# Performance work log

Hardware: AMD Instinct MI355X
Metric: run time of the kernel (lower is better)

## Reference

```python
import jax, jax.numpy as jnp
import numpy as np

MULTIRES = 6          # positional-encoding frequencies (get_embedder)
SKIP_LAYER = 4        # skip_in=(4,) in ImplicitNetwork
BETA = 100.0          # Softplus(beta=100)
INV_SQRT2 = float(1.0 / np.sqrt(2.0))
NUM_NETS = 64         # multi displacement networks (clusters)


def embed(x):
    """NeRF positional embedding: [x, sin(2^k x), cos(2^k x)] for k=0..MULTIRES-1.
    x: [N,3] -> [N, 3 + 3*2*MULTIRES] = [N,39]."""
    outs = [x]
    for i in range(MULTIRES):
        f = float(2.0 ** i)
        outs.append(jnp.sin(f * x))
        outs.append(jnp.cos(f * x))
    return jnp.concatenate(outs, axis=-1)


def softplus100(x):
    # numerically stable softplus with beta=100
    return jnp.logaddexp(0.0, BETA * x) / BETA


def _forward(points,
             iW0, ib0, iW1, ib1, iW2, ib2, iW3, ib3, iW4, ib4,
             iW5, ib5, iW6, ib6, iW7, ib7, iW8, ib8,
             dW0, db0, dW1, db1, dW2, db2, dW3, db3,
             mW0, mb0, mW1, mb1, mW2, mb2):
    N = points.shape[0]
    inp = embed(points)  # [N,39]

    # ---- ImplicitNetwork: 9 linears, softplus(beta=100), skip concat at l=4 ----
    iWs = [iW0, iW1, iW2, iW3, iW4, iW5, iW6, iW7, iW8]
    ibs = [ib0, ib1, ib2, ib3, ib4, ib5, ib6, ib7, ib8]
    x = inp
    for l in range(9):
        if l == SKIP_LAYER:
            x = jnp.concatenate([x, inp], axis=1) * INV_SQRT2  # [N,473+39=512]
        x = x @ iWs[l].T + ibs[l]
        if l < 8:
            x = softplus100(x)
    sdf_feat = x  # [N,257] = sdf (1) + feature vector (256)

    # ---- DisplacementNetwork: 4 linears, ReLU on hidden, Tanh output ----
    xd = inp
    for W, b, last in ((dW0, db0, False), (dW1, db1, False), (dW2, db2, False), (dW3, db3, True)):
        xd = xd @ W.T + b
        xd = jnp.tanh(xd) if last else jax.nn.relu(xd)
    disp = xd  # [N,3]

    # ---- MultiDisplacementNetwork: batched per-cluster MLPs via bmm ----
    xm = inp.reshape(NUM_NETS, -1, inp.shape[1])  # [n, N/n, 39]
    xm = jax.nn.relu(jnp.einsum('nbi,noi->nbo', xm, mW0) + mb0[:, None, :])
    xm = jax.nn.relu(jnp.einsum('nbi,noi->nbo', xm, mW1) + mb1[:, None, :])
    xm = jnp.tanh(jnp.einsum('nbi,noi->nbo', xm, mW2) + mb2[:, None, :])
    mdisp = xm.reshape(N, 3)

    return jnp.concatenate([sdf_feat, disp, mdisp], axis=1)  # [N, 263]


def setup_inputs() -> dict:
    key = jax.random.key(0)
    ks = iter(jax.random.split(key, 80))
    N = 32768
    d = {}
    d['points'] = jax.random.uniform(next(ks), (N, 3), jnp.float32, -1.0, 1.0)

    def mk(out, inn):
        W = jax.random.normal(next(ks), (out, inn), jnp.float32) * (1.0 / np.sqrt(inn))
        b = jax.random.normal(next(ks), (out,), jnp.float32) * 0.01
        return W, b

    impl_shapes = [(512, 39), (512, 512), (512, 512), (473, 512), (512, 512),
                   (512, 512), (512, 512), (512, 512), (257, 512)]
    for l, (o, i) in enumerate(impl_shapes):
        d[f'iW{l}'], d[f'ib{l}'] = mk(o, i)

    disp_shapes = [(512, 39), (512, 512), (512, 512), (3, 512)]
    for l, (o, i) in enumerate(disp_shapes):
        d[f'dW{l}'], d[f'db{l}'] = mk(o, i)

    multi_shapes = [(128, 39), (128, 128), (3, 128)]
    for l, (o, i) in enumerate(multi_shapes):
        W = jax.random.normal(next(ks), (NUM_NETS, o, i), jnp.float32) * (1.0 / np.sqrt(i))
        b = jax.random.normal(next(ks), (NUM_NETS, o), jnp.float32) * 0.01
        d[f'mW{l}'], d[f'mb{l}'] = W, b
    return d


def reference(points,
              iW0, ib0, iW1, ib1, iW2, ib2, iW3, ib3, iW4, ib4,
              iW5, ib5, iW6, ib6, iW7, ib7, iW8, ib8,
              dW0, db0, dW1, db1, dW2, db2, dW3, db3,
              mW0, mb0, mW1, mb1, mW2, mb2):
    return _forward(points,
                    iW0, ib0, iW1, ib1, iW2, ib2, iW3, ib3, iW4, ib4,
                    iW5, ib5, iW6, ib6, iW7, ib7, iW8, ib8,
                    dW0, db0, dW1, db1, dW2, db2, dW3, db3,
                    mW0, mb0, mW1, mb1, mW2, mb2)
```

## Files before the change

kernel.cpp:

```cpp
#include <hip/hip_runtime.h>
#include <hip/hip_bf16.h>
#include <stdint.h>

typedef __attribute__((ext_vector_type(8))) short short8;
typedef __attribute__((ext_vector_type(4))) float floatx4;
typedef __attribute__((ext_vector_type(2))) uint uint2v;

#define INV_SQRT2F 0.70710678118654752440f
#define ROWS 128
#define NT 1024

__device__ ushort g_wbuf[4259840];

__device__ __forceinline__ ushort f2bf(float f) {
    union { float f; uint32_t u; } c; c.f = f;
    uint32_t x = c.u;
    return (ushort)((x + 0x7fffu + ((x >> 16) & 1u)) >> 16);
}
__device__ __forceinline__ uint pk2bf(float a, float b) {
    union { __hip_bfloat162 h; uint u; } c;
    c.h = __float22bfloat162_rn(make_float2(a, b));
    return c.u;
}
__device__ __forceinline__ float softplus100(float x) {
    float z = 100.f * x;
    return fmaxf(x, 0.f) + __logf(1.f + __expf(-fabsf(z))) * 0.01f;
}
__device__ __forceinline__ void bar_lgkm() {
    asm volatile("s_waitcnt lgkmcnt(0)\n\ts_barrier" ::: "memory");
}
__device__ __forceinline__ int fidx(int K32, int row, int ch) {
    return (((row >> 4) * K32 + (ch >> 5)) * 64 + ((ch >> 3) & 3) * 16 + (row & 15)) * 8 + (ch & 7);
}

struct Seg { const float* s; int off, nout, kw, k32, ttot, nclust; };
struct CvtAll { Seg seg[16]; };

__global__ void k_cvt(CvtAll c) {
    Seg sg = c.seg[blockIdx.y];
    ushort* d = g_wbuf + sg.off;
    const int pcs8 = sg.ttot * sg.k32 * 64;
    const int tot8 = pcs8 * sg.nclust;
    const bool vec = ((sg.kw & 7) == 0);
    for (int i8 = blockIdx.x * blockDim.x + threadIdx.x; i8 < tot8;
         i8 += gridDim.x * blockDim.x) {
        int cl = i8 / pcs8;
        int r = i8 - cl * pcs8;
        int t = r / (sg.k32 * 64);
        int r2 = r - t * (sg.k32 * 64);
        int kc = r2 >> 6;
        int lane = r2 & 63;
        int n = t * 16 + (lane & 15);
        int kb = kc * 32 + (lane >> 4) * 8;
        const float* src = sg.s + (size_t)cl * sg.nout * sg.kw;
        short8 v = {0, 0, 0, 0, 0, 0, 0, 0};
        if (n < sg.nout) {
            if (vec && kb + 8 <= sg.kw) {
                const float4* s4 = (const float4*)(src + (size_t)n * sg.kw + kb);
                float4 a = s4[0], b = s4[1];
                v[0] = (short)f2bf(a.x); v[1] = (short)f2bf(a.y);
                v[2] = (short)f2bf(a.z); v[3] = (short)f2bf(a.w);
                v[4] = (short)f2bf(b.x); v[5] = (short)f2bf(b.y);
                v[6] = (short)f2bf(b.z); v[7] = (short)f2bf(b.w);
            } else {
#pragma unroll
                for (int j = 0; j < 8; ++j) {
                    int k = kb + j;
                    if (k < sg.kw) v[j] = (short)f2bf(src[(size_t)n * sg.kw + k]);
                }
            }
        }
        *(short8*)(d + (size_t)i8 * 8) = v;
    }
}

template<int K32OUT>
__device__ void embedR(short* act, const float* pts, int row0, short* inp_sv) {
    for (int idx = threadIdx.x; idx < ROWS * 64; idx += NT) {
        int row = idx >> 6, col = idx & 63;
        float v = 0.f;
        if (col < 39) {
            int comp = (col < 3) ? col : (col - 3) % 3;
            float x = pts[(row0 + row) * 3 + comp];
            if (col < 3) v = x;
            else {
                int b = col - 3; int fi = b / 6; int r = b % 6;
                float a = x * (float)(1 << fi);
                v = (r < 3) ? __sinf(a) : __cosf(a);
            }
        }
        act[fidx(K32OUT, row, col)] = (short)f2bf(v);
        if (inp_sv && col < 39) inp_sv[row * 40 + col] = (short)f2bf(v * INV_SQRT2F);
    }
}

template<int ACT, int K32IN, int K32OUT, bool FULL>
__device__ void layer_mm(short* act, const ushort* __restrict__ Wf,
                         const float* __restrict__ bias, int Nout, float scale,
                         bool toLds, float* gOut, int gCol0, int gRow0)
{
    const int tid = threadIdx.x;
    const int wave = tid >> 6, lane = tid & 63;
    const int wg = wave & 7, mg = wave >> 3;
    const int q = lane >> 4, li = lane & 15;
    const int lane8 = lane * 8;
    const int Ttot = FULL ? 32 : ((Nout + 15) >> 4);

    floatx4 acc[4][4];
#pragma unroll
    for (int i = 0; i < 4; ++i)
#pragma unroll
        for (int m = 0; m < 4; ++m) acc[i][m] = (floatx4){0.f, 0.f, 0.f, 0.f};

    bool tv[4]; const ushort* wb[4];
#pragma unroll
    for (int i = 0; i < 4; ++i) {
        int t = wg * 4 + i;
        tv[i] = FULL ? true : (t < Ttot);
        wb[i] = Wf + (size_t)t * K32IN * 512 + lane8;
    }

    if (FULL || tv[0]) {
        auto loadB = [&](int kc, short8* b) {
#pragma unroll
            for (int i = 0; i < 4; ++i)
                if (FULL || tv[i]) b[i] = *(const short8*)(wb[i] + kc * 512);
        };
        auto step = [&](int kc, short8* b) {
#pragma unroll
            for (int h = 0; h < 2; ++h) {
                short8 afr[2];
#pragma unroll
                for (int m2 = 0; m2 < 2; ++m2)
                    afr[m2] = *(const short8*)
                        &act[((mg * 4 + h * 2 + m2) * K32IN + kc) * 512 + lane8];
                __builtin_amdgcn_s_setprio(1);
#pragma unroll
                for (int i = 0; i < 4; ++i) {
                    if (!(FULL || tv[i])) continue;
#pragma unroll
                    for (int m2 = 0; m2 < 2; ++m2)
                        acc[i][h * 2 + m2] = __builtin_amdgcn_mfma_f32_16x16x32_bf16(
                            b[i], afr[m2], acc[i][h * 2 + m2], 0, 0, 0);
                }
                __builtin_amdgcn_s_setprio(0);
            }
        };

        short8 b0[4], b1[4];
        loadB(0, b0);
#pragma unroll
        for (int kc = 0; kc < K32IN; kc += 2) {
            if (kc + 1 < K32IN) loadB(kc + 1, b1);
            step(kc, b0);
            if (kc + 2 < K32IN) loadB(kc + 2, b0);
            if (kc + 1 < K32IN) step(kc + 1, b1);
        }
    }
    bar_lgkm();
#pragma unroll
    for (int i = 0; i < 4; ++i) {
        if (!(FULL || tv[i])) continue;
        const int nb = (wg * 4 + i) * 16 + q * 4;
        if (!FULL && nb >= Nout) continue;
        const bool fullN = FULL || (nb + 4) <= Nout;
        float bs[4];
        if (fullN) {
            float4 b4 = *(const float4*)(bias + nb);
            bs[0] = b4.x; bs[1] = b4.y; bs[2] = b4.z; bs[3] = b4.w;
        } else {
#pragma unroll
            for (int r = 0; r < 4; ++r) bs[r] = (nb + r < Nout) ? bias[nb + r] : 0.f;
        }
        const int wbase = ((nb >> 5)) * 512 + ((nb >> 3) & 3) * 128 + li * 8 + (nb & 7);
#pragma unroll
        for (int m2 = 0; m2 < 4; ++m2) {
            const int mAbs = mg * 4 + m2;
            const int row = mAbs * 16 + li;
            float v[4];
#pragma unroll
            for (int r = 0; r < 4; ++r) {
                float x = acc[i][m2][r] + bs[r];
                if (ACT == 1) x = softplus100(x);
                else if (ACT == 2) x = fmaxf(x, 0.f);
                else if (ACT == 3) x = tanhf(x);
                v[r] = x * scale;
            }
            if (toLds) {
                if (fullN) {
                    uint2v pk = {pk2bf(v[0], v[1]), pk2bf(v[2], v[3])};
                    *(uint2v*)&act[mAbs * K32OUT * 512 + wbase] = pk;
                } else {
#pragma unroll
                    for (int r = 0; r < 4; ++r)
                        if (nb + r < Nout)
                            act[fidx(K32OUT, row, nb + r)] = (short)f2bf(v[r]);
                }
            } else {
#pragma unroll
                for (int r = 0; r < 4; ++r)
                    if (nb + r < Nout)
                        gOut[(size_t)(gRow0 + row) * 263 + gCol0 + nb + r] = v[r];
            }
        }
    }
}

struct IP { int iw[9]; const float* ib[9]; };
struct DMP { int dw[4]; const float* db[4]; int mw[3]; const float* mb[3]; };
struct AllP { IP ip; DMP dm; };

struct LayerCtx {
    short* act; short* inp_sv; const float* pts; float* out; int row0;
};

__device__ void run_impl(LayerCtx& c, const IP& p) {
    embedR<2>(c.act, c.pts, c.row0, c.inp_sv);
    bar_lgkm();
    layer_mm<1, 2, 16, true>(c.act, g_wbuf + p.iw[0], p.ib[0], 512, 1.f, true, nullptr, 0, 0);
    bar_lgkm();
    layer_mm<1, 16, 16, true>(c.act, g_wbuf + p.iw[1], p.ib[1], 512, 1.f, true, nullptr, 0, 0);
    bar_lgkm();
    layer_mm<1, 16, 16, true>(c.act, g_wbuf + p.iw[2], p.ib[2], 512, 1.f, true, nullptr, 0, 0);
    bar_lgkm();
    layer_mm<1, 16, 16, false>(c.act, g_wbuf + p.iw[3], p.ib[3], 473, INV_SQRT2F, true, nullptr, 0, 0);
    for (int t2 = threadIdx.x; t2 < ROWS * 64; t2 += NT) {
        int row = t2 >> 6, col = t2 & 63;
        if (col < 39) c.act[fidx(16, row, 473 + col)] = c.inp_sv[row * 40 + col];
    }
    bar_lgkm();
    layer_mm<1, 16, 16, true>(c.act, g_wbuf + p.iw[4], p.ib[4], 512, 1.f, true, nullptr, 0, 0);
    bar_lgkm();
    layer_mm<1, 16, 16, true>(c.act, g_wbuf + p.iw[5], p.ib[5], 512, 1.f, true, nullptr, 0, 0);
    bar_lgkm();
    layer_mm<1, 16, 16, true>(c.act, g_wbuf + p.iw[6], p.ib[6], 512, 1.f, true, nullptr, 0, 0);
    bar_lgkm();
    layer_mm<1, 16, 16, true>(c.act, g_wbuf + p.iw[7], p.ib[7], 512, 1.f, true, nullptr, 0, 0);
    bar_lgkm();
    layer_mm<0, 16, 16, false>(c.act, g_wbuf + p.iw[8], p.ib[8], 257, 1.f, false, c.out, 0, c.row0);
}

__device__ void run_dm(LayerCtx& c, const DMP& p, int rpc) {
    const int cl = c.row0 / rpc;
    const ushort* w0 = g_wbuf + p.mw[0] + cl * 8192;
    const ushort* w1 = g_wbuf + p.mw[1] + cl * 16384;
    const ushort* w2 = g_wbuf + p.mw[2] + cl * 2048;
    embedR<2>(c.act, c.pts, c.row0, nullptr);
    bar_lgkm();
    layer_mm<2, 2, 4, false>(c.act, w0, p.mb[0] + cl * 128, 128, 1.f, true, nullptr, 0, 0);
    bar_lgkm();
    layer_mm<2, 4, 4, false>(c.act, w1, p.mb[1] + cl * 128, 128, 1.f, true, nullptr, 0, 0);
    bar_lgkm();
    layer_mm<3, 4, 4, false>(c.act, w2, p.mb[2] + cl * 3, 3, 1.f, false, c.out, 260, c.row0);
    embedR<2>(c.act, c.pts, c.row0, nullptr);
    bar_lgkm();
    layer_mm<2, 2, 16, true>(c.act, g_wbuf + p.dw[0], p.db[0], 512, 1.f, true, nullptr, 0, 0);
    bar_lgkm();
    layer_mm<2, 16, 16, true>(c.act, g_wbuf + p.dw[1], p.db[1], 512, 1.f, true, nullptr, 0, 0);
    bar_lgkm();
    layer_mm<2, 16, 16, true>(c.act, g_wbuf + p.dw[2], p.db[2], 512, 1.f, true, nullptr, 0, 0);
    bar_lgkm();
    layer_mm<3, 16, 16, false>(c.act, g_wbuf + p.dw[3], p.db[3], 3, 1.f, false, c.out, 257, c.row0);
}

__global__ __launch_bounds__(NT, 4) void k_all(const float* __restrict__ pts,
                                               AllP P, float* __restrict__ out,
                                               int rpc) {
    __shared__ __align__(16) short act[ROWS * 512];
    __shared__ short inp_sv[ROWS * 40];
    const int swz = (blockIdx.x & 7) * 32 + (blockIdx.x >> 3);
    LayerCtx c{act, inp_sv, pts, out, swz * ROWS};
    run_impl(c, P.ip);
    run_dm(c, P.dm, rpc);
}

extern "C" void kernel_launch(void* const* d_in, const int* in_sizes, int n_in,
                              void* d_out, int out_size, void* d_ws, size_t ws_size,
                              hipStream_t stream) {
    const float* pts = (const float*)d_in[0];
    float* out = (float*)d_out;
    const int N = in_sizes[0] / 3;
    const int rpc = N / 64;

    const int iN[9] = {512, 512, 512, 473, 512, 512, 512, 512, 257};
    const int iK[9] = {39, 512, 512, 512, 512, 512, 512, 512, 512};
    const int dN[4] = {512, 512, 512, 3};
    const int dK[4] = {39, 512, 512, 512};
    const int mN[3] = {128, 128, 3};
    const int mK[3] = {39, 128, 128};

    CvtAll cv; AllP P;
    int off = 0, seg = 0;
    auto add_seg = [&](const float* src, int nout, int kw, int nclust) -> int {
        int k32 = ((kw + 31) & ~31) / 32;
        int ttot = (nout + 15) >> 4;
        cv.seg[seg].s = src; cv.seg[seg].off = off;
        cv.seg[seg].nout = nout; cv.seg[seg].kw = kw;
        cv.seg[seg].k32 = k32; cv.seg[seg].ttot = ttot; cv.seg[seg].nclust = nclust;
        int my = off;
        off += ttot * k32 * 512 * nclust;
        ++seg;
        return my;
    };
    for (int l = 0; l < 9; ++l) {
        P.ip.iw[l] = add_seg((const float*)d_in[1 + 2 * l], iN[l], iK[l], 1);
        P.ip.ib[l] = (const float*)d_in[2 + 2 * l];
    }
    for (int l = 0; l < 4; ++l) {
        P.dm.dw[l] = add_seg((const float*)d_in[19 + 2 * l], dN[l], dK[l], 1);
        P.dm.db[l] = (const float*)d_in[20 + 2 * l];
    }
    for (int l = 0; l < 3; ++l) {
        P.dm.mw[l] = add_seg((const float*)d_in[27 + 2 * l], mN[l], mK[l], 64);
        P.dm.mb[l] = (const float*)d_in[28 + 2 * l];
    }

    k_cvt<<<dim3(256, 16), 256, 0, stream>>>(cv);
    k_all<<<N / ROWS, NT, 0, stream>>>(pts, P, out, rpc);
}
```

Before: 463.8 us.

## Halve block to 512 threads with larger per-wave MFMA tiles

The fused MLP kernel now runs 8 waves per block instead of 16. Each wave computes 8 output-column tiles by 4 row tiles, where before it computed 4 by 4. The tile-to-wave mapping becomes interleaved (wg + 4*i), and each activation fragment loaded from LDS is reused across 8 weight fragments instead of 4. The aim is fewer LDS reads per MFMA and better register-level reuse, at the cost of doubling the accumulator registers (128 floats) and half the waves to hide latency. The loop's unroll structure also changes, and launch bounds go from (1024,4) to (512,2).

```diff
diff --git a/kernel.cpp b/kernel.cpp
--- a/kernel.cpp
+++ b/kernel.cpp
@@ -8,7 +8,7 @@
 
 #define INV_SQRT2F 0.70710678118654752440f
 #define ROWS 128
-#define NT 1024
+#define NT 512
 
 __device__ ushort g_wbuf[4259840];
 
@@ -101,67 +101,69 @@
 {
     const int tid = threadIdx.x;
     const int wave = tid >> 6, lane = tid & 63;
-    const int wg = wave & 7, mg = wave >> 3;
+    const int wg = wave & 3, mg = wave >> 2;
     const int q = lane >> 4, li = lane & 15;
     const int lane8 = lane * 8;
     const int Ttot = FULL ? 32 : ((Nout + 15) >> 4);
 
-    floatx4 acc[4][4];
-#pragma unroll
-    for (int i = 0; i < 4; ++i)
+    floatx4 acc[8][4];
+#pragma unroll
+    for (int i = 0; i < 8; ++i)
 #pragma unroll
         for (int m = 0; m < 4; ++m) acc[i][m] = (floatx4){0.f, 0.f, 0.f, 0.f};
 
-    bool tv[4]; const ushort* wb[4];
-#pragma unroll
-    for (int i = 0; i < 4; ++i) {
-        int t = wg * 4 + i;
+    bool tv[8]; const ushort* wb[8];
+#pragma unroll
+    for (int i = 0; i < 8; ++i) {
+        int t = wg + 4 * i;
         tv[i] = FULL ? true : (t < Ttot);
         wb[i] = Wf + (size_t)t * K32IN * 512 + lane8;
     }
 
     if (FULL || tv[0]) {
-        auto loadB = [&](int kc, short8* b) {
-#pragma unroll
-            for (int i = 0; i < 4; ++i)
-                if (FULL || tv[i]) b[i] = *(const short8*)(wb[i] + kc * 512);
+        short8 bA[4], bB[4], afr[4];
+        auto loadB4 = [&](int kc, int half, short8* bb) {
+#pragma unroll
+            for (int j = 0; j < 4; ++j) {
+                int i = half * 4 + j;
+                if (FULL || tv[i]) bb[j] = *(const short8*)(wb[i] + kc * 512);
+            }
         };
-        auto step = [&](int kc, short8* b) {
-#pragma unroll
-            for (int h = 0; h < 2; ++h) {
-                short8 afr[2];
-#pragma unroll
-                for (int m2 = 0; m2 < 2; ++m2)
-                    afr[m2] = *(const short8*)
-                        &act[((mg * 4 + h * 2 + m2) * K32IN + kc) * 512 + lane8];
-                __builtin_amdgcn_s_setprio(1);
-#pragma unroll
-                for (int i = 0; i < 4; ++i) {
-                    if (!(FULL || tv[i])) continue;
-#pragma unroll
-                    for (int m2 = 0; m2 < 2; ++m2)
-                        acc[i][h * 2 + m2] = __builtin_amdgcn_mfma_f32_16x16x32_bf16(
-                            b[i], afr[m2], acc[i][h * 2 + m2], 0, 0, 0);
-                }
-                __builtin_amdgcn_s_setprio(0);
-            }
+        auto loadF = [&](int kc) {
+#pragma unroll
+            for (int m2 = 0; m2 < 4; ++m2)
+                afr[m2] = *(const short8*)
+                    &act[((mg * 4 + m2) * K32IN + kc) * 512 + lane8];
         };
-
-        short8 b0[4], b1[4];
-        loadB(0, b0);
-#pragma unroll
-        for (int kc = 0; kc < K32IN; kc += 2) {
-            if (kc + 1 < K32IN) loadB(kc + 1, b1);
-            step(kc, b0);
-            if (kc + 2 < K32IN) loadB(kc + 2, b0);
-            if (kc + 1 < K32IN) step(kc + 1, b1);
-        }
-    }
-    bar_lgkm();
-#pragma unroll
-    for (int i = 0; i < 4; ++i) {
+        auto mmH = [&](short8* bb, int half) {
+            __builtin_amdgcn_s_setprio(1);
+#pragma unroll
+            for (int j = 0; j < 4; ++j) {
+                int i = half * 4 + j;
+                if (!(FULL || tv[i])) continue;
+#pragma unroll
+                for (int m2 = 0; m2 < 4; ++m2)
+                    acc[i][m2] = __builtin_amdgcn_mfma_f32_16x16x32_bf16(
+                        bb[j], afr[m2], acc[i][m2], 0, 0, 0);
+            }
+            __builtin_amdgcn_s_setprio(0);
+        };
+
+        loadB4(0, 0, bA);
+        loadB4(0, 1, bB);
+        for (int kc = 0; kc < K32IN; ++kc) {
+            loadF(kc);
+            mmH(bA, 0);
+            if (kc + 1 < K32IN) loadB4(kc + 1, 0, bA);
+            mmH(bB, 1);
+            if (kc + 1 < K32IN) loadB4(kc + 1, 1, bB);
+        }
+    }
+    bar_lgkm();
+#pragma unroll
+    for (int i = 0; i < 8; ++i) {
         if (!(FULL || tv[i])) continue;
-        const int nb = (wg * 4 + i) * 16 + q * 4;
+        const int nb = (wg + 4 * i) * 16 + q * 4;
         if (!FULL && nb >= Nout) continue;
         const bool fullN = FULL || (nb + 4) <= Nout;
         float bs[4];
@@ -263,7 +265,7 @@
     layer_mm<3, 16, 16, false>(c.act, g_wbuf + p.dw[3], p.db[3], 3, 1.f, false, c.out, 257, c.row0);
 }
 
-__global__ __launch_bounds__(NT, 4) void k_all(const float* __restrict__ pts,
+__global__ __launch_bounds__(NT, 2) void k_all(const float* __restrict__ pts,
                                                AllP P, float* __restrict__ out,
                                                int rpc) {
     __shared__ __align__(16) short act[ROWS * 512];
```

Result: faster. 401.9 us (-13.3%).
